# Kernel optimization log

Hardware: AMD Instinct MI355X
Metric: run time of the kernel (lower is better)

The kernel has to match this reference:

```python
import jax, jax.numpy as jnp
import numpy as np


def setup_inputs() -> dict:
    key = jax.random.key(0)
    ks = jax.random.split(key, 7)
    OUT, IN, K = 4096, 4096, 2048
    U_STORED, VT_STORED = 512, 1024  # int(0.5*(K//2+1)), int(0.5*(IN//2+1))
    return {
        "x": jax.random.normal(ks[0], (1024, IN), dtype=jnp.float32),
        "U_real": jax.random.normal(ks[1], (OUT, U_STORED), dtype=jnp.float32) * 0.01,
        "U_imag": jax.random.normal(ks[2], (OUT, U_STORED), dtype=jnp.float32) * 0.01,
        "S": jax.random.normal(ks[3], (K,), dtype=jnp.float32) * 0.02,
        "Vt_real": jax.random.normal(ks[4], (K, VT_STORED), dtype=jnp.float32) * 0.01,
        "Vt_imag": jax.random.normal(ks[5], (K, VT_STORED), dtype=jnp.float32) * 0.01,
        "bias": jnp.zeros((OUT,), dtype=jnp.float32),
    }


def _decompress(coeffs_real, coeffs_imag, n):
    # Zero-pad truncated rfft coefficients back to n//2+1, then inverse rfft.
    c = jax.lax.complex(coeffs_real, coeffs_imag)
    num_unique = n // 2 + 1
    pad = num_unique - c.shape[-1]
    if pad > 0:
        c = jnp.pad(c, ((0, 0), (0, pad)))
    elif pad < 0:
        c = c[..., :num_unique]
    return jnp.fft.irfft(c, n=n, axis=-1)


def reference(x, U_real, U_imag, S, Vt_real, Vt_imag, bias):
    k_rank = S.shape[0]
    in_features = x.shape[-1]
    U = _decompress(U_real, U_imag, k_rank)            # (out, k)
    Vh = _decompress(Vt_real, Vt_imag, in_features)    # (k, in)
    W = (U * S[None, :]) @ Vh                          # (out, in) reconstructed weight
    return x @ W.T + bias                              # F.linear(x, W, bias)
```

## Files before the change

### kernel.cpp

```cpp
#include <hip/hip_runtime.h>
#include <math.h>
#include <stdint.h>

#define PI2 6.28318530717958647692f

typedef __bf16 bf16x8 __attribute__((ext_vector_type(8)));
typedef float f32x4 __attribute__((ext_vector_type(4)));

typedef __attribute__((address_space(1))) const void gvoid_t;
typedef __attribute__((address_space(3))) void lvoid_t;

__device__ __forceinline__ void g2l16(const void* g, void* l) {
    __builtin_amdgcn_global_load_lds(
        reinterpret_cast<gvoid_t*>(reinterpret_cast<uintptr_t>(g)),
        reinterpret_cast<lvoid_t*>(reinterpret_cast<uintptr_t>(l)),
        16, 0, 0);
}

__device__ __forceinline__ short f2bf(float f) {
    unsigned u = __float_as_uint(f);
    u += 0x7FFFu + ((u >> 16) & 1u);
    return (short)(u >> 16);
}

__device__ __forceinline__ unsigned pack2bf(float a, float b) {
    return (unsigned)(unsigned short)f2bf(a) |
           ((unsigned)(unsigned short)f2bf(b) << 16);
}

__device__ __forceinline__ float bflo(unsigned v) { return __uint_as_float(v << 16); }
__device__ __forceinline__ float bfhi(unsigned v) { return __uint_as_float(v & 0xFFFF0000u); }

__device__ __forceinline__ int xcd_swizzle(int blk, int G) {
    return (blk & 7) * (G >> 3) + (blk >> 3);
}

__global__ __launch_bounds__(256) void aux_all8(
    const float* __restrict__ x,
    const float* __restrict__ Ur, const float* __restrict__ Ui,
    const float* __restrict__ S,
    const float* __restrict__ Vr, const float* __restrict__ Vi,
    short* __restrict__ xe, short* __restrict__ xo,
    short* __restrict__ B1f, short* __restrict__ Vcat,
    short* __restrict__ B2, short* __restrict__ Ucat)
{
    unsigned i8 = (blockIdx.x * 256u + threadIdx.x) * 8u;
    if (i8 < 2097152u) {
        unsigned i = i8;
        int r = i >> 11, j0 = i & 2047;
        const float* xr = x + (size_t)r * 4096 + j0;
        float4 a0 = ((const float4*)xr)[0], a1 = ((const float4*)xr)[1];
        float4 b0 = ((const float4*)(xr + 2048))[0],
               b1 = ((const float4*)(xr + 2048))[1];
        uint4 oe = {pack2bf(a0.x + b0.x, a0.y + b0.y),
                    pack2bf(a0.z + b0.z, a0.w + b0.w),
                    pack2bf(a1.x + b1.x, a1.y + b1.y),
                    pack2bf(a1.z + b1.z, a1.w + b1.w)};
        *(uint4*)(xe + i) = oe;
        uint4 oo = {pack2bf(a0.x - b0.x, a0.y - b0.y),
                    pack2bf(a0.z - b0.z, a0.w - b0.w),
                    pack2bf(a1.x - b1.x, a1.y - b1.y),
                    pack2bf(a1.z - b1.z, a1.w - b1.w)};
        *(uint4*)(xo + i) = oo;
    } else if (i8 < 6291456u) {
        unsigned i = i8 - 2097152u;
        int r = i >> 11, j0 = i & 2047;
        const float inv_n = 1.0f / 4096.0f;
        float v[8];
        if (r < 512) {
            if (r == 0) {
                #pragma unroll
                for (int u = 0; u < 8; ++u) v[u] = inv_n;
            } else {
                #pragma unroll
                for (int u = 0; u < 8; ++u) {
                    int t = (r * (j0 + u)) & 2047;
                    v[u] = 2.0f * inv_n * cosf((float)t * (PI2 / 2048.0f));
                }
            }
        } else if (r < 1024) {
            int m = r - 512;
            #pragma unroll
            for (int u = 0; u < 8; ++u) {
                int t = (m * (j0 + u)) & 2047;
                v[u] = -2.0f * inv_n * sinf((float)t * (PI2 / 2048.0f));
            }
        } else if (r < 1536) {
            int c = 2 * (r - 1024) + 1;
            #pragma unroll
            for (int u = 0; u < 8; ++u) {
                int t = (c * (j0 + u)) & 4095;
                v[u] = 2.0f * inv_n * cosf((float)t * (PI2 / 4096.0f));
            }
        } else {
            int m = 2 * (r - 1536) + 1;
            #pragma unroll
            for (int u = 0; u < 8; ++u) {
                int t = (m * (j0 + u)) & 4095;
                v[u] = -2.0f * inv_n * sinf((float)t * (PI2 / 4096.0f));
            }
        }
        uint4 o = {pack2bf(v[0], v[1]), pack2bf(v[2], v[3]),
                   pack2bf(v[4], v[5]), pack2bf(v[6], v[7])};
        *(uint4*)(B1f + i) = o;
    } else if (i8 < 10485760u) {
        unsigned i = i8 - 6291456u;
        int k = i >> 11, c0 = i & 2047;
        int cls = c0 >> 9, cc0 = c0 & 511;
        const float* src = ((cls & 1) ? Vi : Vr) + (size_t)k * 1024 + 2 * cc0;
        float4 q0 = ((const float4*)src)[0];
        float4 q1 = ((const float4*)src)[1];
        float4 q2 = ((const float4*)src)[2];
        float4 q3 = ((const float4*)src)[3];
        float v[8];
        if ((cls >> 1) == 0) {
            v[0] = q0.x; v[1] = q0.z; v[2] = q1.x; v[3] = q1.z;
            v[4] = q2.x; v[5] = q2.z; v[6] = q3.x; v[7] = q3.z;
        } else {
            v[0] = q0.y; v[1] = q0.w; v[2] = q1.y; v[3] = q1.w;
            v[4] = q2.y; v[5] = q2.w; v[6] = q3.y; v[7] = q3.w;
        }
        uint4 o = {pack2bf(v[0], v[1]), pack2bf(v[2], v[3]),
                   pack2bf(v[4], v[5]), pack2bf(v[6], v[7])};
        *(uint4*)(Vcat + i) = o;
    } else if (i8 < 12582912u) {
        unsigned i = i8 - 10485760u;
        int p = i >> 11, k0 = i & 2047;
        float4 s0 = *(const float4*)(S + k0);
        float4 s1 = *(const float4*)(S + k0 + 4);
        float sv[8] = {s0.x, s0.y, s0.z, s0.w, s1.x, s1.y, s1.z, s1.w};
        const float inv_n = 1.0f / 2048.0f;
        float v[8];
        if (p == 0) {
            #pragma unroll
            for (int u = 0; u < 8; ++u) v[u] = inv_n * sv[u];
        } else if (p < 512) {
            #pragma unroll
            for (int u = 0; u < 8; ++u) {
                int t = (p * (k0 + u)) & 2047;
                v[u] = 2.0f * inv_n * cosf((float)t * (PI2 / 2048.0f)) * sv[u];
            }
        } else {
            int q = p - 512;
            #pragma unroll
            for (int u = 0; u < 8; ++u) {
                int t = (q * (k0 + u)) & 2047;
                v[u] = -2.0f * inv_n * sinf((float)t * (PI2 / 2048.0f)) * sv[u];
            }
        }
        uint4 o = {pack2bf(v[0], v[1]), pack2bf(v[2], v[3]),
                   pack2bf(v[4], v[5]), pack2bf(v[6], v[7])};
        *(uint4*)(B2 + i) = o;
    } else {
        unsigned i = i8 - 12582912u;
        int o_ = i >> 10, c = i & 1023;
        const float* src = (c < 512) ? (Ur + (size_t)o_ * 512 + c)
                                     : (Ui + (size_t)o_ * 512 + (c - 512));
        float4 a = ((const float4*)src)[0], b = ((const float4*)src)[1];
        uint4 o = {pack2bf(a.x, a.y), pack2bf(a.z, a.w),
                   pack2bf(b.x, b.y), pack2bf(b.z, b.w)};
        *(uint4*)(Ucat + i) = o;
    }
}

__device__ __forceinline__ void tile_core(
    const short* __restrict__ A, int lda,
    const short* __restrict__ B, int ldb, int K,
    short* As, short* Bs, int bm, int bn, f32x4 (&acc)[4][4])
{
    const int tid  = threadIdx.x;
    const int wave = tid >> 6;
    const int lane = tid & 63;
    const int wm   = (wave >> 1) << 6;
    const int wn   = (wave & 1) << 6;
    const int l16  = lane & 15;
    const int quad = lane >> 4;
    const int rk   = l16 & 7;

    int aoff[4], boff[4], loff[4];
    #pragma unroll
    for (int p = 0; p < 4; ++p) {
        int L   = p * 256 + wave * 64 + lane;
        int row = L >> 3;
        int swz = (L & 7) ^ (row & 7);
        aoff[p] = (bm + row) * lda + swz * 8;
        boff[p] = (bn + row) * ldb + swz * 8;
        loff[p] = L * 8;
    }

    #pragma unroll
    for (int p = 0; p < 4; ++p) g2l16(A + aoff[p], As + loff[p]);
    #pragma unroll
    for (int p = 0; p < 4; ++p) g2l16(B + boff[p], Bs + loff[p]);
    __syncthreads();

    int cur = 0;
    for (int k0 = 0; k0 < K; k0 += 64) {
        const int nxt = cur ^ 1;
        if (k0 + 64 < K) {
            #pragma unroll
            for (int p = 0; p < 4; ++p)
                g2l16(A + aoff[p] + k0 + 64, As + nxt * 8192 + loff[p]);
            #pragma unroll
            for (int p = 0; p < 4; ++p)
                g2l16(B + boff[p] + k0 + 64, Bs + nxt * 8192 + loff[p]);
        }

        const short* Asc = As + cur * 8192;
        const short* Bsc = Bs + cur * 8192;
        #pragma unroll
        for (int h = 0; h < 2; ++h) {
            const int cs8 = ((((h << 2) | quad) ^ rk) << 3);
            bf16x8 b[4];
            #pragma unroll
            for (int nt = 0; nt < 4; ++nt)
                b[nt] = *(const bf16x8*)(Bsc + (wn + nt * 16 + l16) * 64 + cs8);
            #pragma unroll
            for (int mt = 0; mt < 4; ++mt) {
                bf16x8 a = *(const bf16x8*)(Asc + (wm + mt * 16 + l16) * 64 + cs8);
                #pragma unroll
                for (int nt = 0; nt < 4; ++nt)
                    acc[mt][nt] = __builtin_amdgcn_mfma_f32_16x16x32_bf16(
                        a, b[nt], acc[mt][nt], 0, 0, 0);
            }
        }
        __syncthreads();
        cur = nxt;
    }
}

__device__ __forceinline__ void store_tile_bf16(
    f32x4 (&acc)[4][4], short* __restrict__ C, int ldc, int bm, int bn)
{
    const int tid  = threadIdx.x;
    const int wave = tid >> 6;
    const int lane = tid & 63;
    const int wm   = (wave >> 1) << 6;
    const int wn   = (wave & 1) << 6;
    const int l16  = lane & 15;
    const int quad = lane >> 4;
    #pragma unroll
    for (int nt = 0; nt < 4; ++nt) {
        int col = bn + wn + nt * 16 + l16;
        #pragma unroll
        for (int mt = 0; mt < 4; ++mt) {
            int rowb = bm + wm + mt * 16 + quad * 4;
            #pragma unroll
            for (int r = 0; r < 4; ++r)
                C[(size_t)(rowb + r) * ldc + col] = f2bf(acc[mt][nt][r]);
        }
    }
}

__device__ __forceinline__ void store_frag(
    f32x4 (&acc)[4][4], short* __restrict__ planeTile)
{
    uint4* p = (uint4*)planeTile;
    const int tid = threadIdx.x;
    #pragma unroll
    for (int c = 0; c < 8; ++c) {
        int nt = c >> 1, mt0 = (c & 1) * 2;
        uint4 o = {pack2bf(acc[mt0][nt][0],     acc[mt0][nt][1]),
                   pack2bf(acc[mt0][nt][2],     acc[mt0][nt][3]),
                   pack2bf(acc[mt0 + 1][nt][0], acc[mt0 + 1][nt][1]),
                   pack2bf(acc[mt0 + 1][nt][2], acc[mt0 + 1][nt][3])};
        p[c * 256 + tid] = o;
    }
}

template <bool OUT_F32>
__device__ __forceinline__ void reduce_unit(
    const short* __restrict__ P, size_t planeU4, int SK,
    int tile, int c, int tilesX, void* __restrict__ Out, int ldc,
    const float* __restrict__ bias)
{
    const int bm = (tile / tilesX) << 7;
    const int bn = (tile % tilesX) << 7;
    const int tid  = threadIdx.x;
    const int wave = tid >> 6;
    const int lane = tid & 63;
    const int wm   = (wave >> 1) << 6;
    const int wn   = (wave & 1) << 6;
    const int l16  = lane & 15;
    const int quad = lane >> 4;
    const int nt   = c >> 1, mt0 = (c & 1) * 2;

    const uint4* P4 = (const uint4*)P;
    const size_t base = (size_t)tile * 2048 + (size_t)c * 256 + tid;
    float f[8] = {0, 0, 0, 0, 0, 0, 0, 0};
    for (int z = 0; z < SK; ++z) {
        uint4 v = P4[(size_t)z * planeU4 + base];
        f[0] += bflo(v.x); f[1] += bfhi(v.x);
        f[2] += bflo(v.y); f[3] += bfhi(v.y);
        f[4] += bflo(v.z); f[5] += bfhi(v.z);
        f[6] += bflo(v.w); f[7] += bfhi(v.w);
    }
    const int col = bn + wn + nt * 16 + l16;
    float bv = 0.f;
    if (OUT_F32) bv = bias[col];
    #pragma unroll
    for (int j = 0; j < 8; ++j) {
        int mt  = mt0 + (j >> 2);
        int row = bm + wm + mt * 16 + quad * 4 + (j & 3);
        if (OUT_F32)
            ((float*)Out)[(size_t)row * ldc + col] = f[j] + bv;
        else
            ((short*)Out)[(size_t)row * ldc + col] = f2bf(f[j]);
    }
}

__global__ __launch_bounds__(256, 2) void gemm_s1f(
    const short* __restrict__ xe, const short* __restrict__ xo,
    const short* __restrict__ B1f, short* __restrict__ P)
{
    __shared__ __align__(16) short As[2 * 128 * 64];
    __shared__ __align__(16) short Bs[2 * 128 * 64];

    f32x4 acc[4][4];
    #pragma unroll
    for (int i = 0; i < 4; ++i)
        #pragma unroll
        for (int j = 0; j < 4; ++j)
            acc[i][j] = (f32x4){0.f, 0.f, 0.f, 0.f};

    const int u    = xcd_swizzle((int)blockIdx.x, (int)gridDim.x);
    const int z    = u >> 7;
    const int tile = u & 127;
    const int tx   = tile & 15, ty = tile >> 4;
    const bool odd = (tx & 8) != 0;
    const short* A = (odd ? xo : xe) + (size_t)z * 512;
    const short* B = B1f + (odd ? (size_t)1024 * 2048 : 0) + (size_t)z * 512;
    const int bm   = ty << 7;
    const int bn   = (tx & 7) << 7;

    tile_core(A, 2048, B, 2048, 512, As, Bs, bm, bn, acc);
    store_frag(acc, P + (size_t)z * 2097152 + (size_t)tile * 16384);
}

__global__ __launch_bounds__(256, 2) void gemm_sk_frag(
    const short* __restrict__ A, int lda,
    const short* __restrict__ B, int ldb,
    short* __restrict__ P, size_t planeShorts, int Kpart,
    int tileShift, int tilesXShift)
{
    __shared__ __align__(16) short As[2 * 128 * 64];
    __shared__ __align__(16) short Bs[2 * 128 * 64];

    f32x4 acc[4][4];
    #pragma unroll
    for (int i = 0; i < 4; ++i)
        #pragma unroll
        for (int j = 0; j < 4; ++j)
            acc[i][j] = (f32x4){0.f, 0.f, 0.f, 0.f};

    const int u    = xcd_swizzle((int)blockIdx.x, (int)gridDim.x);
    const int z    = u >> tileShift;
    const int tile = u & ((1 << tileShift) - 1);
    const int bm   = (tile >> tilesXShift) << 7;
    const int bn   = (tile & ((1 << tilesXShift) - 1)) << 7;

    tile_core(A + (size_t)z * Kpart, lda, B + (size_t)z * Kpart, ldb, Kpart,
              As, Bs, bm, bn, acc);
    store_frag(acc, P + (size_t)z * planeShorts + (size_t)tile * 16384);
}

template <bool OUT_F32>
__global__ __launch_bounds__(256) void reduce_frag(
    const short* __restrict__ P, size_t planeShorts, int SK,
    int tilesX, void* __restrict__ Out, int ldc,
    const float* __restrict__ bias)
{
    reduce_unit<OUT_F32>(P, planeShorts >> 3, SK,
                         (int)(blockIdx.x >> 3), (int)(blockIdx.x & 7),
                         tilesX, Out, ldc, bias);
}

template <bool OUT_F32>
__global__ __launch_bounds__(256, 2) void gemm_direct(
    const short* __restrict__ A, int lda,
    const short* __restrict__ B, int ldb,
    void* __restrict__ Cv, int ldc,
    const float* __restrict__ bias, int K)
{
    __shared__ __align__(16) short As[2 * 128 * 64];
    __shared__ __align__(16) short Bs[2 * 128 * 64];

    f32x4 acc[4][4];
    #pragma unroll
    for (int i = 0; i < 4; ++i)
        #pragma unroll
        for (int j = 0; j < 4; ++j)
            acc[i][j] = (f32x4){0.f, 0.f, 0.f, 0.f};

    const int bm = blockIdx.y << 7;
    const int bn = blockIdx.x << 7;
    tile_core(A, lda, B, ldb, K, As, Bs, bm, bn, acc);

    const int tid  = threadIdx.x;
    const int wave = tid >> 6;
    const int lane = tid & 63;
    const int wm   = (wave >> 1) << 6;
    const int wn   = (wave & 1) << 6;
    const int l16  = lane & 15;
    const int quad = lane >> 4;

    if (OUT_F32) {
        float* C = (float*)Cv;
        #pragma unroll
        for (int nt = 0; nt < 4; ++nt) {
            int col = bn + wn + nt * 16 + l16;
            float bv = bias ? bias[col] : 0.f;
            #pragma unroll
            for (int mt = 0; mt < 4; ++mt) {
                int rowb = bm + wm + mt * 16 + quad * 4;
                #pragma unroll
                for (int r = 0; r < 4; ++r)
                    C[(size_t)(rowb + r) * ldc + col] = acc[mt][nt][r] + bv;
            }
        }
    } else {
        store_tile_bf16(acc, (short*)Cv, ldc, bm, bn);
    }
}

extern "C" void kernel_launch(void* const* d_in, const int* in_sizes, int n_in,
                              void* d_out, int out_size, void* d_ws, size_t ws_size,
                              hipStream_t stream) {
    const float* x    = (const float*)d_in[0];
    const float* Ur   = (const float*)d_in[1];
    const float* Ui   = (const float*)d_in[2];
    const float* S    = (const float*)d_in[3];
    const float* Vr   = (const float*)d_in[4];
    const float* Vi   = (const float*)d_in[5];
    const float* bias = (const float*)d_in[6];
    float* out = (float*)d_out;

    short* ws   = (short*)d_ws;
    short* xe   = ws;
    short* xo   = xe   + (size_t)1024 * 2048;
    short* B1f  = xo   + (size_t)1024 * 2048;
    short* Vcat = B1f  + (size_t)2048 * 2048;
    short* B2   = Vcat + (size_t)2048 * 2048;
    short* Ucat = B2   + (size_t)1024 * 2048;
    short* Xp   = Ucat + (size_t)4096 * 1024;
    short* T1   = Xp   + (size_t)1024 * 2048;
    short* Gm   = T1   + (size_t)1024 * 2048;
    short* Pp   = Gm   + (size_t)1024 * 1024;

    const size_t need = (size_t)((char*)(Pp + (size_t)8388608) - (char*)d_ws);

    aux_all8<<<dim3(8192), 256, 0, stream>>>(
        x, Ur, Ui, S, Vr, Vi, xe, xo, B1f, Vcat, B2, Ucat);

    if (ws_size >= need) {
        gemm_s1f<<<dim3(512), 256, 0, stream>>>(xe, xo, B1f, Pp);
        reduce_frag<false><<<dim3(1024), 256, 0, stream>>>(
            Pp, (size_t)2097152, 4, 16, Xp, 2048, nullptr);

        gemm_sk_frag<<<dim3(512), 256, 0, stream>>>(
            Xp, 2048, Vcat, 2048, Pp, (size_t)2097152, 512, 7, 4);
        reduce_frag<false><<<dim3(1024), 256, 0, stream>>>(
            Pp, (size_t)2097152, 4, 16, T1, 2048, nullptr);

        gemm_sk_frag<<<dim3(512), 256, 0, stream>>>(
            T1, 2048, B2, 2048, Pp, (size_t)1048576, 256, 6, 3);
        reduce_frag<false><<<dim3(512), 256, 0, stream>>>(
            Pp, (size_t)1048576, 8, 8, Gm, 1024, nullptr);

        gemm_sk_frag<<<dim3(512), 256, 0, stream>>>(
            Gm, 1024, Ucat, 1024, Pp, (size_t)4194304, 512, 8, 5);
        reduce_frag<true><<<dim3(2048), 256, 0, stream>>>(
            Pp, (size_t)4194304, 2, 32, out, 4096, bias);
    } else {
        gemm_direct<false><<<dim3(8, 8), 256, 0, stream>>>(
            xe, 2048, B1f, 2048, Xp, 2048, nullptr, 2048);
        gemm_direct<false><<<dim3(8, 8), 256, 0, stream>>>(
            xo, 2048, B1f + (size_t)1024 * 2048, 2048, Xp + 1024, 2048,
            nullptr, 2048);
        gemm_direct<false><<<dim3(16, 8), 256, 0, stream>>>(
            Xp, 2048, Vcat, 2048, T1, 2048, nullptr, 2048);
        gemm_direct<false><<<dim3(8, 8), 256, 0, stream>>>(
            T1, 2048, B2, 2048, Gm, 1024, nullptr, 2048);
        gemm_direct<true><<<dim3(32, 8), 256, 0, stream>>>(
            Gm, 1024, Ucat, 1024, out, 4096, bias, 1024);
    }
}
```

Measured before the change: 185.2 us.

## Replace split-K GEMMs plus reduction kernels with direct single-pass GEMMs

Result: slower. 194.5 us (+5.0%).

```diff
diff --git a/kernel.cpp b/kernel.cpp
--- a/kernel.cpp
+++ b/kernel.cpp
@@ -27,9 +27,6 @@
     return (unsigned)(unsigned short)f2bf(a) |
            ((unsigned)(unsigned short)f2bf(b) << 16);
 }
-
-__device__ __forceinline__ float bflo(unsigned v) { return __uint_as_float(v << 16); }
-__device__ __forceinline__ float bfhi(unsigned v) { return __uint_as_float(v & 0xFFFF0000u); }
 
 __device__ __forceinline__ int xcd_swizzle(int blk, int G) {
     return (blk & 7) * (G >> 3) + (blk >> 3);
@@ -252,66 +249,9 @@
     }
 }
 
-__device__ __forceinline__ void store_frag(
-    f32x4 (&acc)[4][4], short* __restrict__ planeTile)
-{
-    uint4* p = (uint4*)planeTile;
-    const int tid = threadIdx.x;
-    #pragma unroll
-    for (int c = 0; c < 8; ++c) {
-        int nt = c >> 1, mt0 = (c & 1) * 2;
-        uint4 o = {pack2bf(acc[mt0][nt][0],     acc[mt0][nt][1]),
-                   pack2bf(acc[mt0][nt][2],     acc[mt0][nt][3]),
-                   pack2bf(acc[mt0 + 1][nt][0], acc[mt0 + 1][nt][1]),
-                   pack2bf(acc[mt0 + 1][nt][2], acc[mt0 + 1][nt][3])};
-        p[c * 256 + tid] = o;
-    }
-}
-
-template <bool OUT_F32>
-__device__ __forceinline__ void reduce_unit(
-    const short* __restrict__ P, size_t planeU4, int SK,
-    int tile, int c, int tilesX, void* __restrict__ Out, int ldc,
-    const float* __restrict__ bias)
-{
-    const int bm = (tile / tilesX) << 7;
-    const int bn = (tile % tilesX) << 7;
-    const int tid  = threadIdx.x;
-    const int wave = tid >> 6;
-    const int lane = tid & 63;
-    const int wm   = (wave >> 1) << 6;
-    const int wn   = (wave & 1) << 6;
-    const int l16  = lane & 15;
-    const int quad = lane >> 4;
-    const int nt   = c >> 1, mt0 = (c & 1) * 2;
-
-    const uint4* P4 = (const uint4*)P;
-    const size_t base = (size_t)tile * 2048 + (size_t)c * 256 + tid;
-    float f[8] = {0, 0, 0, 0, 0, 0, 0, 0};
-    for (int z = 0; z < SK; ++z) {
-        uint4 v = P4[(size_t)z * planeU4 + base];
-        f[0] += bflo(v.x); f[1] += bfhi(v.x);
-        f[2] += bflo(v.y); f[3] += bfhi(v.y);
-        f[4] += bflo(v.z); f[5] += bfhi(v.z);
-        f[6] += bflo(v.w); f[7] += bfhi(v.w);
-    }
-    const int col = bn + wn + nt * 16 + l16;
-    float bv = 0.f;
-    if (OUT_F32) bv = bias[col];
-    #pragma unroll
-    for (int j = 0; j < 8; ++j) {
-        int mt  = mt0 + (j >> 2);
-        int row = bm + wm + mt * 16 + quad * 4 + (j & 3);
-        if (OUT_F32)
-            ((float*)Out)[(size_t)row * ldc + col] = f[j] + bv;
-        else
-            ((short*)Out)[(size_t)row * ldc + col] = f2bf(f[j]);
-    }
-}
-
-__global__ __launch_bounds__(256, 2) void gemm_s1f(
+__global__ __launch_bounds__(256, 2) void gemm_s1f_dir(
     const short* __restrict__ xe, const short* __restrict__ xo,
-    const short* __restrict__ B1f, short* __restrict__ P)
+    const short* __restrict__ B1f, short* __restrict__ Xp)
 {
     __shared__ __align__(16) short As[2 * 128 * 64];
     __shared__ __align__(16) short Bs[2 * 128 * 64];
@@ -324,24 +264,22 @@
             acc[i][j] = (f32x4){0.f, 0.f, 0.f, 0.f};
 
     const int u    = xcd_swizzle((int)blockIdx.x, (int)gridDim.x);
-    const int z    = u >> 7;
-    const int tile = u & 127;
-    const int tx   = tile & 15, ty = tile >> 4;
+    const int tx   = u & 15, ty = u >> 4;
     const bool odd = (tx & 8) != 0;
-    const short* A = (odd ? xo : xe) + (size_t)z * 512;
-    const short* B = B1f + (odd ? (size_t)1024 * 2048 : 0) + (size_t)z * 512;
+    const short* A = odd ? xo : xe;
+    const short* B = B1f + (odd ? (size_t)1024 * 2048 : 0);
     const int bm   = ty << 7;
     const int bn   = (tx & 7) << 7;
 
-    tile_core(A, 2048, B, 2048, 512, As, Bs, bm, bn, acc);
-    store_frag(acc, P + (size_t)z * 2097152 + (size_t)tile * 16384);
-}
-
-__global__ __launch_bounds__(256, 2) void gemm_sk_frag(
+    tile_core(A, 2048, B, 2048, 2048, As, Bs, bm, bn, acc);
+    store_tile_bf16(acc, Xp, 2048, bm, bn + (odd ? 1024 : 0));
+}
+
+template <bool OUT_F32>
+__global__ __launch_bounds__(256, 2) void gemm_dir(
     const short* __restrict__ A, int lda,
-    const short* __restrict__ B, int ldb,
-    short* __restrict__ P, size_t planeShorts, int Kpart,
-    int tileShift, int tilesXShift)
+    const short* __restrict__ B, int ldb, int K, int tilesXShift,
+    void* __restrict__ Cv, int ldc, const float* __restrict__ bias)
 {
     __shared__ __align__(16) short As[2 * 128 * 64];
     __shared__ __align__(16) short Bs[2 * 128 * 64];
@@ -353,63 +291,25 @@
         for (int j = 0; j < 4; ++j)
             acc[i][j] = (f32x4){0.f, 0.f, 0.f, 0.f};
 
-    const int u    = xcd_swizzle((int)blockIdx.x, (int)gridDim.x);
-    const int z    = u >> tileShift;
-    const int tile = u & ((1 << tileShift) - 1);
-    const int bm   = (tile >> tilesXShift) << 7;
-    const int bn   = (tile & ((1 << tilesXShift) - 1)) << 7;
-
-    tile_core(A + (size_t)z * Kpart, lda, B + (size_t)z * Kpart, ldb, Kpart,
-              As, Bs, bm, bn, acc);
-    store_frag(acc, P + (size_t)z * planeShorts + (size_t)tile * 16384);
-}
-
-template <bool OUT_F32>
-__global__ __launch_bounds__(256) void reduce_frag(
-    const short* __restrict__ P, size_t planeShorts, int SK,
-    int tilesX, void* __restrict__ Out, int ldc,
-    const float* __restrict__ bias)
-{
-    reduce_unit<OUT_F32>(P, planeShorts >> 3, SK,
-                         (int)(blockIdx.x >> 3), (int)(blockIdx.x & 7),
-                         tilesX, Out, ldc, bias);
-}
-
-template <bool OUT_F32>
-__global__ __launch_bounds__(256, 2) void gemm_direct(
-    const short* __restrict__ A, int lda,
-    const short* __restrict__ B, int ldb,
-    void* __restrict__ Cv, int ldc,
-    const float* __restrict__ bias, int K)
-{
-    __shared__ __align__(16) short As[2 * 128 * 64];
-    __shared__ __align__(16) short Bs[2 * 128 * 64];
-
-    f32x4 acc[4][4];
-    #pragma unroll
-    for (int i = 0; i < 4; ++i)
-        #pragma unroll
-        for (int j = 0; j < 4; ++j)
-            acc[i][j] = (f32x4){0.f, 0.f, 0.f, 0.f};
-
-    const int bm = blockIdx.y << 7;
-    const int bn = blockIdx.x << 7;
+    const int u  = xcd_swizzle((int)blockIdx.x, (int)gridDim.x);
+    const int bm = (u >> tilesXShift) << 7;
+    const int bn = (u & ((1 << tilesXShift) - 1)) << 7;
+
     tile_core(A, lda, B, ldb, K, As, Bs, bm, bn, acc);
 
-    const int tid  = threadIdx.x;
-    const int wave = tid >> 6;
-    const int lane = tid & 63;
-    const int wm   = (wave >> 1) << 6;
-    const int wn   = (wave & 1) << 6;
-    const int l16  = lane & 15;
-    const int quad = lane >> 4;
-
     if (OUT_F32) {
+        const int tid  = threadIdx.x;
+        const int wave = tid >> 6;
+        const int lane = tid & 63;
+        const int wm   = (wave >> 1) << 6;
+        const int wn   = (wave & 1) << 6;
+        const int l16  = lane & 15;
+        const int quad = lane >> 4;
         float* C = (float*)Cv;
         #pragma unroll
         for (int nt = 0; nt < 4; ++nt) {
             int col = bn + wn + nt * 16 + l16;
-            float bv = bias ? bias[col] : 0.f;
+            float bv = bias[col];
             #pragma unroll
             for (int mt = 0; mt < 4; ++mt) {
                 int rowb = bm + wm + mt * 16 + quad * 4;
@@ -445,43 +345,18 @@
     short* Xp   = Ucat + (size_t)4096 * 1024;
     short* T1   = Xp   + (size_t)1024 * 2048;
     short* Gm   = T1   + (size_t)1024 * 2048;
-    short* Pp   = Gm   + (size_t)1024 * 1024;
-
-    const size_t need = (size_t)((char*)(Pp + (size_t)8388608) - (char*)d_ws);
 
     aux_all8<<<dim3(8192), 256, 0, stream>>>(
         x, Ur, Ui, S, Vr, Vi, xe, xo, B1f, Vcat, B2, Ucat);
 
-    if (ws_size >= need) {
-        gemm_s1f<<<dim3(512), 256, 0, stream>>>(xe, xo, B1f, Pp);
-        reduce_frag<false><<<dim3(1024), 256, 0, stream>>>(
-            Pp, (size_t)2097152, 4, 16, Xp, 2048, nullptr);
-
-        gemm_sk_frag<<<dim3(512), 256, 0, stream>>>(
-            Xp, 2048, Vcat, 2048, Pp, (size_t)2097152, 512, 7, 4);
-        reduce_frag<false><<<dim3(1024), 256, 0, stream>>>(
-            Pp, (size_t)2097152, 4, 16, T1, 2048, nullptr);
-
-        gemm_sk_frag<<<dim3(512), 256, 0, stream>>>(
-            T1, 2048, B2, 2048, Pp, (size_t)1048576, 256, 6, 3);
-        reduce_frag<false><<<dim3(512), 256, 0, stream>>>(
-            Pp, (size_t)1048576, 8, 8, Gm, 1024, nullptr);
-
-        gemm_sk_frag<<<dim3(512), 256, 0, stream>>>(
-            Gm, 1024, Ucat, 1024, Pp, (size_t)4194304, 512, 8, 5);
-        reduce_frag<true><<<dim3(2048), 256, 0, stream>>>(
-            Pp, (size_t)4194304, 2, 32, out, 4096, bias);
-    } else {
-        gemm_direct<false><<<dim3(8, 8), 256, 0, stream>>>(
-            xe, 2048, B1f, 2048, Xp, 2048, nullptr, 2048);
-        gemm_direct<false><<<dim3(8, 8), 256, 0, stream>>>(
-            xo, 2048, B1f + (size_t)1024 * 2048, 2048, Xp + 1024, 2048,
-            nullptr, 2048);
-        gemm_direct<false><<<dim3(16, 8), 256, 0, stream>>>(
-            Xp, 2048, Vcat, 2048, T1, 2048, nullptr, 2048);
-        gemm_direct<false><<<dim3(8, 8), 256, 0, stream>>>(
-            T1, 2048, B2, 2048, Gm, 1024, nullptr, 2048);
-        gemm_direct<true><<<dim3(32, 8), 256, 0, stream>>>(
-            Gm, 1024, Ucat, 1024, out, 4096, bias, 1024);
-    }
-}
+    gemm_s1f_dir<<<dim3(128), 256, 0, stream>>>(xe, xo, B1f, Xp);
+
+    gemm_dir<false><<<dim3(128), 256, 0, stream>>>(
+        Xp, 2048, Vcat, 2048, 2048, 4, T1, 2048, nullptr);
+
+    gemm_dir<false><<<dim3(64), 256, 0, stream>>>(
+        T1, 2048, B2, 2048, 2048, 3, Gm, 1024, nullptr);
+
+    gemm_dir<true><<<dim3(256), 256, 0, stream>>>(
+        Gm, 1024, Ucat, 1024, 1024, 5, out, 4096, bias);
+}
```

## Reassociate Vh chain so weight-side GEMM runs concurrently with x transform

Applied to the files above, without the earlier changes.

Measured after the change: 224.4 us. 21.1% more time.

```diff
diff --git a/kernel.cpp b/kernel.cpp
--- a/kernel.cpp
+++ b/kernel.cpp
@@ -41,7 +41,7 @@
     const float* __restrict__ S,
     const float* __restrict__ Vr, const float* __restrict__ Vi,
     short* __restrict__ xe, short* __restrict__ xo,
-    short* __restrict__ B1f, short* __restrict__ Vcat,
+    short* __restrict__ B1f, short* __restrict__ VcatT,
     short* __restrict__ B2, short* __restrict__ Ucat)
 {
     unsigned i8 = (blockIdx.x * 256u + threadIdx.x) * 8u;
@@ -104,25 +104,19 @@
                    pack2bf(v[4], v[5]), pack2bf(v[6], v[7])};
         *(uint4*)(B1f + i) = o;
     } else if (i8 < 10485760u) {
-        unsigned i = i8 - 6291456u;
-        int k = i >> 11, c0 = i & 2047;
-        int cls = c0 >> 9, cc0 = c0 & 511;
-        const float* src = ((cls & 1) ? Vi : Vr) + (size_t)k * 1024 + 2 * cc0;
-        float4 q0 = ((const float4*)src)[0];
-        float4 q1 = ((const float4*)src)[1];
-        float4 q2 = ((const float4*)src)[2];
-        float4 q3 = ((const float4*)src)[3];
+        unsigned e = i8 - 6291456u;
+        int t_lin = e >> 3;
+        int f   = t_lin >> 8;
+        int kk0 = (t_lin & 255) << 3;
+        int cls = f >> 9, cc = f & 511;
+        const float* src = ((cls & 1) ? Vi : Vr) + 2 * cc + (cls >> 1);
         float v[8];
-        if ((cls >> 1) == 0) {
-            v[0] = q0.x; v[1] = q0.z; v[2] = q1.x; v[3] = q1.z;
-            v[4] = q2.x; v[5] = q2.z; v[6] = q3.x; v[7] = q3.z;
-        } else {
-            v[0] = q0.y; v[1] = q0.w; v[2] = q1.y; v[3] = q1.w;
-            v[4] = q2.y; v[5] = q2.w; v[6] = q3.y; v[7] = q3.w;
-        }
+        #pragma unroll
+        for (int u = 0; u < 8; ++u)
+            v[u] = src[(size_t)(kk0 + u) * 1024];
         uint4 o = {pack2bf(v[0], v[1]), pack2bf(v[2], v[3]),
                    pack2bf(v[4], v[5]), pack2bf(v[6], v[7])};
-        *(uint4*)(Vcat + i) = o;
+        *(uint4*)(VcatT + e) = o;
     } else if (i8 < 12582912u) {
         unsigned i = i8 - 10485760u;
         int p = i >> 11, k0 = i & 2047;
@@ -309,9 +303,11 @@
     }
 }
 
-__global__ __launch_bounds__(256, 2) void gemm_s1f(
+__global__ __launch_bounds__(256, 2) void gemm_s1w2(
     const short* __restrict__ xe, const short* __restrict__ xo,
-    const short* __restrict__ B1f, short* __restrict__ P)
+    const short* __restrict__ B1f,
+    const short* __restrict__ B2, const short* __restrict__ VcatT,
+    short* __restrict__ P, short* __restrict__ PW)
 {
     __shared__ __align__(16) short As[2 * 128 * 64];
     __shared__ __align__(16) short Bs[2 * 128 * 64];
@@ -323,18 +319,45 @@
         for (int j = 0; j < 4; ++j)
             acc[i][j] = (f32x4){0.f, 0.f, 0.f, 0.f};
 
-    const int u    = xcd_swizzle((int)blockIdx.x, (int)gridDim.x);
-    const int z    = u >> 7;
-    const int tile = u & 127;
-    const int tx   = tile & 15, ty = tile >> 4;
-    const bool odd = (tx & 8) != 0;
-    const short* A = (odd ? xo : xe) + (size_t)z * 512;
-    const short* B = B1f + (odd ? (size_t)1024 * 2048 : 0) + (size_t)z * 512;
-    const int bm   = ty << 7;
-    const int bn   = (tx & 7) << 7;
-
-    tile_core(A, 2048, B, 2048, 512, As, Bs, bm, bn, acc);
-    store_frag(acc, P + (size_t)z * 2097152 + (size_t)tile * 16384);
+    const int raw = (int)blockIdx.x;
+    if (raw < 512) {
+        const int u    = xcd_swizzle(raw, 512);
+        const int z    = u >> 7;
+        const int tile = u & 127;
+        const int tx   = tile & 15, ty = tile >> 4;
+        const bool odd = (tx & 8) != 0;
+        const short* A = (odd ? xo : xe) + (size_t)z * 512;
+        const short* B = B1f + (odd ? (size_t)1024 * 2048 : 0) + (size_t)z * 512;
+        const int bm   = ty << 7;
+        const int bn   = (tx & 7) << 7;
+
+        tile_core(A, 2048, B, 2048, 512, As, Bs, bm, bn, acc);
+        store_frag(acc, P + (size_t)z * 2097152 + (size_t)tile * 16384);
+    } else {
+        const int u    = xcd_swizzle(raw - 512, 512);
+        const int z    = u >> 7;
+        const int tile = u & 127;
+        const int bm   = (tile >> 4) << 7;
+        const int bn   = (tile & 15) << 7;
+
+        tile_core(B2 + (size_t)z * 512, 2048, VcatT + (size_t)z * 512, 2048,
+                  512, As, Bs, bm, bn, acc);
+        store_frag(acc, PW + (size_t)z * 2097152 + (size_t)tile * 16384);
+    }
+}
+
+__global__ __launch_bounds__(256) void reduce_s1w2(
+    const short* __restrict__ P, const short* __restrict__ PW,
+    short* __restrict__ Xp, short* __restrict__ W2)
+{
+    const int b   = (int)blockIdx.x;
+    const int sub = b & 1023;
+    if (b < 1024)
+        reduce_unit<false>(P,  (size_t)2097152 >> 3, 4, sub >> 3, sub & 7,
+                           16, Xp, 2048, nullptr);
+    else
+        reduce_unit<false>(PW, (size_t)2097152 >> 3, 4, sub >> 3, sub & 7,
+                           16, W2, 2048, nullptr);
 }
 
 __global__ __launch_bounds__(256, 2) void gemm_sk_frag(
@@ -421,6 +444,32 @@
     } else {
         store_tile_bf16(acc, (short*)Cv, ldc, bm, bn);
     }
+}
+
+__global__ __launch_bounds__(256, 2) void gemm_s1f_dir(
+    const short* __restrict__ xe, const short* __restrict__ xo,
+    const short* __restrict__ B1f, short* __restrict__ Xp)
+{
+    __shared__ __align__(16) short As[2 * 128 * 64];
+    __shared__ __align__(16) short Bs[2 * 128 * 64];
+
+    f32x4 acc[4][4];
+    #pragma unroll
+    for (int i = 0; i < 4; ++i)
+        #pragma unroll
+        for (int j = 0; j < 4; ++j)
+            acc[i][j] = (f32x4){0.f, 0.f, 0.f, 0.f};
+
+    const int u    = (int)blockIdx.x;
+    const int tx   = u & 15, ty = u >> 4;
+    const bool odd = (tx & 8) != 0;
+    const short* A = odd ? xo : xe;
+    const short* B = B1f + (odd ? (size_t)1024 * 2048 : 0);
+    const int bm   = ty << 7;
+    const int bn   = (tx & 7) << 7;
+
+    tile_core(A, 2048, B, 2048, 2048, As, Bs, bm, bn, acc);
+    store_tile_bf16(acc, Xp, 2048, bm, bn + (odd ? 1024 : 0));
 }
 
 extern "C" void kernel_launch(void* const* d_in, const int* in_sizes, int n_in,
@@ -435,35 +484,31 @@
     const float* bias = (const float*)d_in[6];
     float* out = (float*)d_out;
 
-    short* ws   = (short*)d_ws;
-    short* xe   = ws;
-    short* xo   = xe   + (size_t)1024 * 2048;
-    short* B1f  = xo   + (size_t)1024 * 2048;
-    short* Vcat = B1f  + (size_t)2048 * 2048;
-    short* B2   = Vcat + (size_t)2048 * 2048;
-    short* Ucat = B2   + (size_t)1024 * 2048;
-    short* Xp   = Ucat + (size_t)4096 * 1024;
-    short* T1   = Xp   + (size_t)1024 * 2048;
-    short* Gm   = T1   + (size_t)1024 * 2048;
-    short* Pp   = Gm   + (size_t)1024 * 1024;
-
-    const size_t need = (size_t)((char*)(Pp + (size_t)8388608) - (char*)d_ws);
+    short* ws    = (short*)d_ws;
+    short* xe    = ws;
+    short* xo    = xe    + (size_t)1024 * 2048;
+    short* B1f   = xo    + (size_t)1024 * 2048;
+    short* VcatT = B1f   + (size_t)2048 * 2048;
+    short* B2    = VcatT + (size_t)2048 * 2048;
+    short* Ucat  = B2    + (size_t)1024 * 2048;
+    short* Xp    = Ucat  + (size_t)4096 * 1024;
+    short* W2    = Xp    + (size_t)1024 * 2048;
+    short* Gm    = W2    + (size_t)1024 * 2048;
+    short* Pp    = Gm    + (size_t)1024 * 1024;
+    short* PW    = Pp    + (size_t)8388608;
+
+    const size_t need = (size_t)((char*)(PW + (size_t)8388608) - (char*)d_ws);
 
     aux_all8<<<dim3(8192), 256, 0, stream>>>(
-        x, Ur, Ui, S, Vr, Vi, xe, xo, B1f, Vcat, B2, Ucat);
+        x, Ur, Ui, S, Vr, Vi, xe, xo, B1f, VcatT, B2, Ucat);
 
     if (ws_size >= need) {
-        gemm_s1f<<<dim3(512), 256, 0, stream>>>(xe, xo, B1f, Pp);
-        reduce_frag<false><<<dim3(1024), 256, 0, stream>>>(
-            Pp, (size_t)2097152, 4, 16, Xp, 2048, nullptr);
+        gemm_s1w2<<<dim3(1024), 256, 0, stream>>>(
+            xe, xo, B1f, B2, VcatT, Pp, PW);
+        reduce_s1w2<<<dim3(2048), 256, 0, stream>>>(Pp, PW, Xp, W2);
 
         gemm_sk_frag<<<dim3(512), 256, 0, stream>>>(
-            Xp, 2048, Vcat, 2048, Pp, (size_t)2097152, 512, 7, 4);
-        reduce_frag<false><<<dim3(1024), 256, 0, stream>>>(
-            Pp, (size_t)2097152, 4, 16, T1, 2048, nullptr);
-
-        gemm_sk_frag<<<dim3(512), 256, 0, stream>>>(
-            T1, 2048, B2, 2048, Pp, (size_t)1048576, 256, 6, 3);
+            Xp, 2048, W2, 2048, Pp, (size_t)1048576, 256, 6, 3);
         reduce_frag<false><<<dim3(512), 256, 0, stream>>>(
             Pp, (size_t)1048576, 8, 8, Gm, 1024, nullptr);
 
@@ -472,15 +517,11 @@
         reduce_frag<true><<<dim3(2048), 256, 0, stream>>>(
             Pp, (size_t)4194304, 2, 32, out, 4096, bias);
     } else {
+        gemm_s1f_dir<<<dim3(128), 256, 0, stream>>>(xe, xo, B1f, Xp);
+        gemm_direct<false><<<dim3(16, 8), 256, 0, stream>>>(
+            B2, 2048, VcatT, 2048, W2, 2048, nullptr, 2048);
         gemm_direct<false><<<dim3(8, 8), 256, 0, stream>>>(
-            xe, 2048, B1f, 2048, Xp, 2048, nullptr, 2048);
-        gemm_direct<false><<<dim3(8, 8), 256, 0, stream>>>(
-            xo, 2048, B1f + (size_t)1024 * 2048, 2048, Xp + 1024, 2048,
-            nullptr, 2048);
-        gemm_direct<false><<<dim3(16, 8), 256, 0, stream>>>(
-            Xp, 2048, Vcat, 2048, T1, 2048, nullptr, 2048);
-        gemm_direct<false><<<dim3(8, 8), 256, 0, stream>>>(
-            T1, 2048, B2, 2048, Gm, 1024, nullptr, 2048);
+            Xp, 2048, W2, 2048, Gm, 1024, nullptr, 2048);
         gemm_direct<true><<<dim3(32, 8), 256, 0, stream>>>(
             Gm, 1024, Ucat, 1024, out, 4096, bias, 1024);
     }
```
